# Optimization experiments

Measured on AMD Instinct MI355X. Metric: run time of the kernel, lower is better.

The kernel has to match this reference:

```python
import jax, jax.numpy as jnp
import numpy as np

B, N, C, NH = 4, 2304, 256, 8
HD = C // NH            # head dim = 32
HS = WS = 48            # H = W = sqrt(N)
RADIUS = 3.0
MLP_HID = 4 * C
SCALE = HD ** (-0.5)
NEG = -1e9              # stands in for -inf (identical softmax up to fp eps)
EPS = 1e-6


def spatial_mask():
    # get_spatial_mask: cdist of (y, x) grid coords, -inf where dist > radius
    yy, xx = jnp.meshgrid(jnp.arange(HS), jnp.arange(WS), indexing='ij')
    coords = jnp.stack([yy, xx], -1).reshape(-1, 2).astype(jnp.float32)  # [N, 2]
    d2 = jnp.sum((coords[:, None, :] - coords[None, :, :]) ** 2, -1)     # [N, N]
    return jnp.where(d2 > RADIUS * RADIUS, NEG, 0.0)


def layernorm(x, g, b):
    mu = jnp.mean(x, -1, keepdims=True)
    var = jnp.mean((x - mu) ** 2, -1, keepdims=True)
    return (x - mu) * jax.lax.rsqrt(var + EPS) * g + b


def setup_inputs() -> dict:
    key = jax.random.key(0)
    ks = jax.random.split(key, 16)
    s = 0.02
    return {
        'x':    jax.random.normal(ks[0], (B, N, C), jnp.float32),
        'x_kv': jax.random.normal(ks[1], (B, N, C), jnp.float32),
        'Wq': jax.random.normal(ks[2], (C, C), jnp.float32) * s,
        'bq': jnp.zeros((C,), jnp.float32),
        'Wk': jax.random.normal(ks[3], (C, C), jnp.float32) * s,
        'bk': jnp.zeros((C,), jnp.float32),
        'Wv': jax.random.normal(ks[4], (C, C), jnp.float32) * s,
        'bv': jnp.zeros((C,), jnp.float32),
        'Wp': jax.random.normal(ks[5], (C, C), jnp.float32) * s,
        'bp': jnp.zeros((C,), jnp.float32),
        'g1': jnp.ones((C,), jnp.float32),
        'b1': jnp.zeros((C,), jnp.float32),
        'g2': jnp.ones((C,), jnp.float32),
        'b2': jnp.zeros((C,), jnp.float32),
        'W1': jax.random.normal(ks[6], (C, MLP_HID), jnp.float32) * s,
        'bm1': jnp.zeros((MLP_HID,), jnp.float32),
        'W2': jax.random.normal(ks[7], (MLP_HID, C), jnp.float32) * s,
        'bm2': jnp.zeros((C,), jnp.float32),
    }


def reference(x, x_kv, Wq, bq, Wk, bk, Wv, bv, Wp, bp,
              g1, b1, g2, b2, W1, bm1, W2, bm2):
    mask = spatial_mask()                                  # [N, N]
    h = layernorm(x, g1, b1)
    hkv = layernorm(x_kv, g1, b1)
    q = (h @ Wq + bq).reshape(B, N, NH, HD)
    k = (hkv @ Wk + bk).reshape(B, N, NH, HD)
    v = (hkv @ Wv + bv).reshape(B, N, NH, HD)
    scores = jnp.einsum('bqhd,bkhd->bhqk', q, k) * SCALE + mask
    attn = jax.nn.softmax(scores, axis=-1)
    out = jnp.einsum('bhqk,bkhd->bqhd', attn, v).reshape(B, N, C)
    x = x + out @ Wp + bp
    m = layernorm(x, g2, b2)
    x = x + jax.nn.gelu(m @ W1 + bm1, approximate=False) @ W2 + bm2
    return x
```

## Files before the change

### kernel.cpp

```cpp
#include <hip/hip_runtime.h>
#include <hip/hip_fp16.h>
#include <math.h>

#define BB 4
#define NN 2304
#define CC 256
#define HS 48
#define HID 1024
#define BNROWS (BB * NN)
#define ATTN_SCALE 0.17677669529663687f

typedef _Float16 f16;
typedef __attribute__((ext_vector_type(2))) _Float16 h2;
typedef __attribute__((ext_vector_type(8))) _Float16 h8;
typedef __attribute__((ext_vector_type(4))) float f4;

#define GLLS16(g, l)                                                        \
    __builtin_amdgcn_global_load_lds(                                       \
        (const __attribute__((address_space(1))) unsigned int*)(g),         \
        (__attribute__((address_space(3))) unsigned int*)(l), 16, 0, 0)

#define WAIT_VM0()   asm volatile("s_waitcnt vmcnt(0)" ::: "memory")
#define WAIT_LGKM0() asm volatile("s_waitcnt lgkmcnt(0)" ::: "memory")

static __device__ __forceinline__ float wave_sum64(float v) {
    v += __shfl_xor(v, 32, 64);
    v += __shfl_xor(v, 16, 64);
    v += __shfl_xor(v, 8, 64);
    v += __shfl_xor(v, 4, 64);
    v += __shfl_xor(v, 2, 64);
    v += __shfl_xor(v, 1, 64);
    return v;
}

__global__ __launch_bounds__(256) void prep_kernel(
    const float* __restrict__ Wq, const float* __restrict__ Wk,
    const float* __restrict__ Wv, const float* __restrict__ Wp,
    const float* __restrict__ W1, const float* __restrict__ W2,
    const float* __restrict__ bq, const float* __restrict__ bk,
    const float* __restrict__ bv,
    f16* __restrict__ WqkvT, f16* __restrict__ WpT,
    f16* __restrict__ W1T, f16* __restrict__ W2T, float* __restrict__ bqkv)
{
    int bx = blockIdx.x;
    if (bx == 768) {
        const int t = threadIdx.x;
        bqkv[t]       = bq[t];
        bqkv[t + 256] = bk[t];
        bqkv[t + 512] = bv[t];
        return;
    }
    __shared__ float tt[32][33];
    const float* src; f16* dst; int K, N;
    if (bx < 64)        { src = Wq; dst = WqkvT;             K = 256;  N = 256; }
    else if (bx < 128)  { src = Wk; dst = WqkvT + 65536;     K = 256;  N = 256;  bx -= 64; }
    else if (bx < 192)  { src = Wv; dst = WqkvT + 131072;    K = 256;  N = 256;  bx -= 128; }
    else if (bx < 256)  { src = Wp; dst = WpT;               K = 256;  N = 256;  bx -= 192; }
    else if (bx < 512)  { src = W1; dst = W1T;               K = 256;  N = 1024; bx -= 256; }
    else                { src = W2; dst = W2T;               K = 1024; N = 256;  bx -= 512; }
    const int tN = N >> 5;
    const int kt = bx / tN, nt = bx - kt * tN;
    const int rr = threadIdx.x >> 5, cc = threadIdx.x & 31;
#pragma unroll
    for (int j = 0; j < 4; ++j)
        tt[rr + 8 * j][cc] = src[(size_t)(kt * 32 + rr + 8 * j) * N + nt * 32 + cc];
    __syncthreads();
#pragma unroll
    for (int j = 0; j < 4; ++j)
        dst[(size_t)(nt * 32 + rr + 8 * j) * K + kt * 32 + cc] = (f16)tt[cc][rr + 8 * j];
}

__global__ __launch_bounds__(256) void ln1_kernel(
    const float* __restrict__ x, const float* __restrict__ xkv,
    const float* __restrict__ g, const float* __restrict__ be,
    f16* __restrict__ hq, f16* __restrict__ hkv)
{
    const int r = blockIdx.x * 4 + (threadIdx.x >> 6);
    const int lane = threadIdx.x & 63;
    const float* src; f16* dst;
    if (r < BNROWS) { src = x + (size_t)r * CC;             dst = hq + (size_t)r * CC; }
    else { src = xkv + (size_t)(r - BNROWS) * CC; dst = hkv + (size_t)(r - BNROWS) * CC; }
    const float4 v = ((const float4*)src)[lane];
    const float mu = wave_sum64(v.x + v.y + v.z + v.w) * (1.0f / CC);
    const float d0 = v.x - mu, d1 = v.y - mu, d2 = v.z - mu, d3 = v.w - mu;
    const float var = wave_sum64(d0 * d0 + d1 * d1 + d2 * d2 + d3 * d3) * (1.0f / CC);
    const float rs = rsqrtf(var + 1e-6f);
    const float4 g4 = ((const float4*)g)[lane];
    const float4 b4 = ((const float4*)be)[lane];
    h2 o01 = (h2){(f16)(d0 * rs * g4.x + b4.x), (f16)(d1 * rs * g4.y + b4.y)};
    h2 o23 = (h2){(f16)(d2 * rs * g4.z + b4.z), (f16)(d3 * rs * g4.w + b4.w)};
    ((h2*)dst)[lane * 2] = o01;
    ((h2*)dst)[lane * 2 + 1] = o23;
}

__global__ __launch_bounds__(256) void ln2_kernel(
    const f16* __restrict__ x1, const float* __restrict__ g,
    const float* __restrict__ be, f16* __restrict__ m2)
{
    const int r = blockIdx.x * 4 + (threadIdx.x >> 6);
    const int lane = threadIdx.x & 63;
    const f16* src = x1 + (size_t)r * CC;
    const h2 a01 = ((const h2*)src)[lane * 2];
    const h2 a23 = ((const h2*)src)[lane * 2 + 1];
    const float v0 = (float)a01[0], v1 = (float)a01[1];
    const float v2 = (float)a23[0], v3 = (float)a23[1];
    const float mu = wave_sum64(v0 + v1 + v2 + v3) * (1.0f / CC);
    const float d0 = v0 - mu, d1 = v1 - mu, d2 = v2 - mu, d3 = v3 - mu;
    const float var = wave_sum64(d0 * d0 + d1 * d1 + d2 * d2 + d3 * d3) * (1.0f / CC);
    const float rs = rsqrtf(var + 1e-6f);
    const float4 g4 = ((const float4*)g)[lane];
    const float4 b4 = ((const float4*)be)[lane];
    f16* dst = m2 + (size_t)r * CC;
    h2 o01 = (h2){(f16)(d0 * rs * g4.x + b4.x), (f16)(d1 * rs * g4.y + b4.y)};
    h2 o23 = (h2){(f16)(d2 * rs * g4.z + b4.z), (f16)(d3 * rs * g4.w + b4.w)};
    ((h2*)dst)[lane * 2] = o01;
    ((h2*)dst)[lane * 2 + 1] = o23;
}

template <int TM, bool GELU, int RESID, bool OUTF32, bool QKV>
__global__ __launch_bounds__(256, 4) void gemm_wave(
    const f16* __restrict__ Aq, const f16* __restrict__ Akv,
    const f16* __restrict__ Bt, const float* __restrict__ bias,
    const void* __restrict__ resid, void* __restrict__ out1,
    void* __restrict__ outkv, int M, int N, int K)
{
    constexpr int AT = TM / 16;
    constexpr int AELEM = TM * 32;
    __shared__ f16 lds[4 * (AELEM + 2048)];
    const int tid = threadIdx.x;
    const int wid = tid >> 6, lane = tid & 63;
    const int ln15 = lane & 15, quad = lane >> 4;
    f16* Al = lds + wid * (AELEM + 2048);
    f16* Bl = Al + AELEM;
    const int n0 = blockIdx.x * 64;
    const int m0 = (blockIdx.y * 4 + wid) * TM;
    const f16* Ap = QKV ? (n0 < 256 ? Aq : Akv) : Aq;

    const int jr = lane >> 2, js = lane & 3;
    size_t ga[AT], gb[4];
#pragma unroll
    for (int i = 0; i < AT; ++i) {
        const int r = i * 16 + jr;
        const int q = (js - (r >> 1)) & 3;
        ga[i] = (size_t)(m0 + r) * K + q * 8;
    }
#pragma unroll
    for (int i = 0; i < 4; ++i) {
        const int r = i * 16 + jr;
        const int q = (js - (r >> 1)) & 3;
        gb[i] = (size_t)(n0 + r) * K + q * 8;
    }
    int aoff[AT], boff[4];
#pragma unroll
    for (int mt = 0; mt < AT; ++mt) {
        const int r = mt * 16 + ln15;
        aoff[mt] = (r * 4 + ((quad + (r >> 1)) & 3)) * 16;
    }
#pragma unroll
    for (int nt = 0; nt < 4; ++nt) {
        const int r = nt * 16 + ln15;
        boff[nt] = (r * 4 + ((quad + (r >> 1)) & 3)) * 16;
    }

    f4 acc[AT][4];
#pragma unroll
    for (int i = 0; i < AT; ++i)
#pragma unroll
        for (int j = 0; j < 4; ++j) acc[i][j] = (f4){0.f, 0.f, 0.f, 0.f};

    for (int k0 = 0; k0 < K; k0 += 32) {
        if (k0) WAIT_LGKM0();
#pragma unroll
        for (int i = 0; i < AT; ++i)
            GLLS16(Ap + ga[i] + k0, Al + i * 512);
#pragma unroll
        for (int i = 0; i < 4; ++i)
            GLLS16(Bt + gb[i] + k0, Bl + i * 512);
        WAIT_VM0();
        h8 bF[4], aF[AT];
#pragma unroll
        for (int nt = 0; nt < 4; ++nt)
            bF[nt] = *(const h8*)((const char*)Bl + boff[nt]);
#pragma unroll
        for (int mt = 0; mt < AT; ++mt)
            aF[mt] = *(const h8*)((const char*)Al + aoff[mt]);
#pragma unroll
        for (int mt = 0; mt < AT; ++mt)
#pragma unroll
            for (int nt = 0; nt < 4; ++nt)
                acc[mt][nt] = __builtin_amdgcn_mfma_f32_16x16x32_f16(
                    aF[mt], bF[nt], acc[mt][nt], 0, 0, 0);
    }

#pragma unroll
    for (int nt = 0; nt < 4; ++nt) {
        const int gn = n0 + nt * 16 + ln15;
        const float bs = bias[gn];
#pragma unroll
        for (int mt = 0; mt < AT; ++mt) {
#pragma unroll
            for (int r = 0; r < 4; ++r) {
                const int gm = m0 + mt * 16 + quad * 4 + r;
                float v = acc[mt][nt][r] + bs;
                if (GELU) v = 0.5f * v * (1.0f + erff(v * 0.70710678118654752f));
                if (RESID == 1) v += ((const float*)resid)[(size_t)gm * N + gn];
                if (RESID == 2) v += (float)((const f16*)resid)[(size_t)gm * N + gn];
                if (QKV) {
                    if (gn < 256) ((f16*)out1)[(size_t)gm * 256 + gn] = (f16)v;
                    else ((f16*)outkv)[(size_t)gm * 512 + (gn - 256)] = (f16)v;
                } else if (OUTF32) {
                    ((float*)out1)[(size_t)gm * N + gn] = v;
                } else {
                    ((f16*)out1)[(size_t)gm * N + gn] = (f16)v;
                }
            }
        }
    }
}

__device__ __constant__ int ATT_DY[29] = {
    -3, -2, -2, -2, -2, -2, -1, -1, -1, -1, -1, 0, 0, 0, 0,
    0, 0, 0, 1, 1, 1, 1, 1, 2, 2, 2, 2, 2, 3};
__device__ __constant__ int ATT_DX[29] = {
    0, -2, -1, 0, 1, 2, -2, -1, 0, 1, 2, -3, -2, -1, 0,
    1, 2, 3, -2, -1, 0, 1, 2, -2, -1, 0, 1, 2, 0};

__global__ __launch_bounds__(128) void attn_tile_kernel(
    const f16* __restrict__ qf, const f16* __restrict__ kvf,
    f16* __restrict__ ao)
{
    __shared__ f16 ks[196][66];
    __shared__ f16 vs[196][66];
    const int tile = blockIdx.x, hp = blockIdx.y, b = blockIdx.z;
    const int ty0 = (tile / 6) * 8, tx0 = (tile - (tile / 6) * 6) * 8;
    const int tid = threadIdx.x;

    for (int idx = tid; idx < 196 * 16; idx += 128) {
        const int r = idx >> 4, seg = idx & 15;
        const int gy = ty0 - 3 + r / 14, gx = tx0 - 3 + (r - (r / 14) * 14);
        uint4 val = {0u, 0u, 0u, 0u};
        if ((unsigned)gy < HS && (unsigned)gx < HS) {
            const size_t rowb = ((size_t)b * NN + gy * HS + gx) * 512;
            const int ch = (seg < 8) ? (hp * 64 + seg * 8)
                                     : (256 + hp * 64 + (seg - 8) * 8);
            val = *(const uint4*)&kvf[rowb + ch];
        }
        f16* dstp = (seg < 8) ? &ks[r][(seg & 7) * 8] : &vs[r][(seg & 7) * 8];
        ((unsigned int*)dstp)[0] = val.x;
        ((unsigned int*)dstp)[1] = val.y;
        ((unsigned int*)dstp)[2] = val.z;
        ((unsigned int*)dstp)[3] = val.w;
    }
    __syncthreads();

    const int q = tid & 63, hh = tid >> 6;
    const int qy = q >> 3, qx = q & 7;
    const size_t qrow = (size_t)b * NN + (ty0 + qy) * HS + tx0 + qx;
    const f16* qp = qf + qrow * CC + hp * 64 + hh * 32;
    uint4 qa[4];
#pragma unroll
    for (int i = 0; i < 4; ++i) qa[i] = ((const uint4*)qp)[i];
    const h2* q2 = (const h2*)qa;

    float s[29];
#pragma unroll
    for (int n = 0; n < 29; ++n) {
        const int dy = ATT_DY[n], dx = ATT_DX[n];
        const int r = (qy + 3 + dy) * 14 + qx + 3 + dx;
        const bool valid = (unsigned)(ty0 + qy + dy) < HS &&
                           (unsigned)(tx0 + qx + dx) < HS;
        float a = 0.0f;
        const h2* kp = (const h2*)&ks[r][hh * 32];
#pragma unroll
        for (int i = 0; i < 16; ++i)
            a = __builtin_amdgcn_fdot2(q2[i], kp[i], a, false);
        s[n] = valid ? a * ATTN_SCALE : -1e30f;
    }
    float m = s[0];
#pragma unroll
    for (int n = 1; n < 29; ++n) m = fmaxf(m, s[n]);
    float l = 0.0f;
#pragma unroll
    for (int n = 0; n < 29; ++n) { s[n] = __expf(s[n] - m); l += s[n]; }
    h2 a2[16];
#pragma unroll
    for (int i = 0; i < 16; ++i) a2[i] = (h2){(f16)0.f, (f16)0.f};
#pragma unroll
    for (int n = 0; n < 29; ++n) {
        const int dy = ATT_DY[n], dx = ATT_DX[n];
        const int r = (qy + 3 + dy) * 14 + qx + 3 + dx;
        const f16 pn = (f16)s[n];
        const h2 ph = (h2){pn, pn};
        const h2* vp = (const h2*)&vs[r][hh * 32];
#pragma unroll
        for (int i = 0; i < 16; ++i) a2[i] += ph * vp[i];
    }
    const float inv = 1.0f / l;
    uint4 ov[4];
    f16* oh = (f16*)ov;
#pragma unroll
    for (int i = 0; i < 16; ++i) {
        oh[2 * i]     = (f16)((float)a2[i][0] * inv);
        oh[2 * i + 1] = (f16)((float)a2[i][1] * inv);
    }
    uint4* dst = (uint4*)(ao + qrow * CC + hp * 64 + hh * 32);
#pragma unroll
    for (int i = 0; i < 4; ++i) dst[i] = ov[i];
}

extern "C" void kernel_launch(void* const* d_in, const int* in_sizes, int n_in,
                              void* d_out, int out_size, void* d_ws, size_t ws_size,
                              hipStream_t stream) {
    const float* x    = (const float*)d_in[0];
    const float* x_kv = (const float*)d_in[1];
    const float* Wq   = (const float*)d_in[2];
    const float* bq   = (const float*)d_in[3];
    const float* Wk   = (const float*)d_in[4];
    const float* bk   = (const float*)d_in[5];
    const float* Wv   = (const float*)d_in[6];
    const float* bv   = (const float*)d_in[7];
    const float* Wp   = (const float*)d_in[8];
    const float* bp   = (const float*)d_in[9];
    const float* g1   = (const float*)d_in[10];
    const float* b1   = (const float*)d_in[11];
    const float* g2   = (const float*)d_in[12];
    const float* b2   = (const float*)d_in[13];
    const float* W1   = (const float*)d_in[14];
    const float* bm1  = (const float*)d_in[15];
    const float* W2   = (const float*)d_in[16];
    const float* bm2  = (const float*)d_in[17];
    float* outp = (float*)d_out;

    f16* wsh = (f16*)d_ws;
    f16* WqkvT = wsh;
    f16* WpT   = wsh + 196608;
    f16* W1T   = wsh + 262144;
    f16* W2T   = wsh + 524288;
    float* bqkv = (float*)(wsh + 786432);
    f16* hq    = wsh + 787968;
    f16* hkv   = wsh + 3147264;
    f16* qf    = wsh + 5506560;
    f16* kvf   = wsh + 7865856;
    f16* ao    = hq;
    f16* x1    = hkv;
    f16* m2    = qf;
    f16* hidF  = kvf;
    const bool fused = ws_size >= (size_t)17303040 * sizeof(f16);

    prep_kernel<<<769, 256, 0, stream>>>(Wq, Wk, Wv, Wp, W1, W2, bq, bk, bv,
                                         WqkvT, WpT, W1T, W2T, bqkv);
    ln1_kernel<<<2 * BNROWS / 4, 256, 0, stream>>>(x, x_kv, g1, b1, hq, hkv);
    gemm_wave<64, false, 0, false, true><<<dim3(12, 36), 256, 0, stream>>>(
        hq, hkv, WqkvT, bqkv, nullptr, qf, kvf, BNROWS, 768, CC);
    attn_tile_kernel<<<dim3(36, 4, BB), 128, 0, stream>>>(qf, kvf, ao);
    gemm_wave<32, false, 1, false, false><<<dim3(4, 72), 256, 0, stream>>>(
        ao, nullptr, WpT, bp, x, x1, nullptr, BNROWS, CC, CC);
    ln2_kernel<<<BNROWS / 4, 256, 0, stream>>>(x1, g2, b2, m2);
    if (fused) {
        gemm_wave<64, true, 0, false, false><<<dim3(16, 36), 256, 0, stream>>>(
            m2, nullptr, W1T, bm1, nullptr, hidF, nullptr, BNROWS, HID, CC);
        gemm_wave<32, false, 2, true, false><<<dim3(4, 72), 256, 0, stream>>>(
            hidF, nullptr, W2T, bm2, x1, outp, nullptr, BNROWS, CC, HID);
    } else {
        for (int b = 0; b < BB; ++b) {
            const size_t off = (size_t)b * NN * CC;
            gemm_wave<64, true, 0, false, false><<<dim3(16, 9), 256, 0, stream>>>(
                m2 + off, nullptr, W1T, bm1, nullptr, hidF, nullptr, NN, HID, CC);
            gemm_wave<32, false, 2, true, false><<<dim3(4, 18), 256, 0, stream>>>(
                hidF, nullptr, W2T, bm2, x1 + off, outp + off, nullptr, NN, CC, HID);
        }
    }
    (void)in_sizes; (void)n_in; (void)out_size;
}
```

Baseline: 196.9 us.

## Fuse all stages into one persistent cooperative megakernel with grid syncs

Replaces the chain of separate kernel launches (weight prep, LN1, QKV GEMM, attention, projection, LN2, MLP GEMMs) with a single cooperative kernel of 256 blocks x 512 threads that steps through the phases and calls grid.sync between them. The GEMMs become a per-wave loop over 32x64 tiles with a software-prefetched LDS load. Attention now reads K/V straight from global memory per thread instead of staging a tile in shared memory. This removes launch gaps but adds grid-wide barrier costs, drops the LDS reuse in attention, and uses small GEMM tiles. The workspace layout no longer aliases buffers and needs more memory, and the fallback for small workspaces is removed.

```diff
diff --git a/kernel.cpp b/kernel.cpp
--- a/kernel.cpp
+++ b/kernel.cpp
@@ -1,6 +1,9 @@
 #include <hip/hip_runtime.h>
 #include <hip/hip_fp16.h>
+#include <hip/hip_cooperative_groups.h>
 #include <math.h>
+
+namespace cg = cooperative_groups;
 
 #define BB 4
 #define NN 2304
@@ -9,6 +12,7 @@
 #define HID 1024
 #define BNROWS (BB * NN)
 #define ATTN_SCALE 0.17677669529663687f
+#define NWAVES 2048
 
 typedef _Float16 f16;
 typedef __attribute__((ext_vector_type(2))) _Float16 h2;
@@ -19,9 +23,15 @@
     __builtin_amdgcn_global_load_lds(                                       \
         (const __attribute__((address_space(1))) unsigned int*)(g),         \
         (__attribute__((address_space(3))) unsigned int*)(l), 16, 0, 0)
-
 #define WAIT_VM0()   asm volatile("s_waitcnt vmcnt(0)" ::: "memory")
 #define WAIT_LGKM0() asm volatile("s_waitcnt lgkmcnt(0)" ::: "memory")
+
+__device__ __constant__ int ATT_DY[29] = {
+    -3, -2, -2, -2, -2, -2, -1, -1, -1, -1, -1, 0, 0, 0, 0,
+    0, 0, 0, 1, 1, 1, 1, 1, 2, 2, 2, 2, 2, 3};
+__device__ __constant__ int ATT_DX[29] = {
+    0, -2, -1, 0, 1, 2, -2, -1, 0, 1, 2, -3, -2, -1, 0,
+    1, 2, 3, -2, -1, 0, 1, 2, -2, -1, 0, 1, 2, 0};
 
 static __device__ __forceinline__ float wave_sum64(float v) {
     v += __shfl_xor(v, 32, 64);
@@ -33,279 +43,303 @@
     return v;
 }
 
-__global__ __launch_bounds__(256) void prep_kernel(
+template <bool GELU, int RESID, bool OUTF32, bool QKV>
+static __device__ void gemm_phase(
+    f16* slot, int gw,
+    const f16* __restrict__ Aq, const f16* __restrict__ Akv,
+    const f16* __restrict__ Bt, const float* __restrict__ bias,
+    const void* __restrict__ resid, void* __restrict__ out1,
+    void* __restrict__ outkv, int Mtiles, int Ntiles, int N, int K)
+{
+    const int lane = threadIdx.x & 63;
+    const int ln15 = lane & 15, quad = lane >> 4;
+    const int jr = lane >> 2, js = lane & 3;
+    f16* Al = slot;
+    f16* Bl = slot + 1024;
+    const int T = Mtiles * Ntiles;
+
+    for (int t = gw; t < T; t += NWAVES) {
+        const int n0 = (t % Ntiles) * 64;
+        const int m0 = (t / Ntiles) * 32;
+        const f16* Ap = QKV ? (n0 < 256 ? Aq : Akv) : Aq;
+
+        size_t ga[2], gb[4];
+#pragma unroll
+        for (int i = 0; i < 2; ++i) {
+            const int r = i * 16 + jr;
+            const int q = (js - (r >> 1)) & 3;
+            ga[i] = (size_t)(m0 + r) * K + q * 8;
+        }
+#pragma unroll
+        for (int i = 0; i < 4; ++i) {
+            const int r = i * 16 + jr;
+            const int q = (js - (r >> 1)) & 3;
+            gb[i] = (size_t)(n0 + r) * K + q * 8;
+        }
+        int aoff[2], boff[4];
+#pragma unroll
+        for (int mt = 0; mt < 2; ++mt) {
+            const int r = mt * 16 + ln15;
+            aoff[mt] = (r * 4 + ((quad + (r >> 1)) & 3)) * 16;
+        }
+#pragma unroll
+        for (int nt = 0; nt < 4; ++nt) {
+            const int r = nt * 16 + ln15;
+            boff[nt] = (r * 4 + ((quad + (r >> 1)) & 3)) * 16;
+        }
+
+        f4 acc[2][4];
+#pragma unroll
+        for (int i = 0; i < 2; ++i)
+#pragma unroll
+            for (int j = 0; j < 4; ++j) acc[i][j] = (f4){0.f, 0.f, 0.f, 0.f};
+
+#pragma unroll
+        for (int i = 0; i < 2; ++i) GLLS16(Ap + ga[i], Al + i * 512);
+#pragma unroll
+        for (int i = 0; i < 4; ++i) GLLS16(Bt + gb[i], Bl + i * 512);
+
+        for (int k0 = 0; k0 < K; k0 += 32) {
+            WAIT_VM0();
+            h8 aF[2], bF[4];
+#pragma unroll
+            for (int nt = 0; nt < 4; ++nt)
+                bF[nt] = *(const h8*)((const char*)Bl + boff[nt]);
+#pragma unroll
+            for (int mt = 0; mt < 2; ++mt)
+                aF[mt] = *(const h8*)((const char*)Al + aoff[mt]);
+            WAIT_LGKM0();
+            if (k0 + 32 < K) {
+#pragma unroll
+                for (int i = 0; i < 2; ++i)
+                    GLLS16(Ap + ga[i] + k0 + 32, Al + i * 512);
+#pragma unroll
+                for (int i = 0; i < 4; ++i)
+                    GLLS16(Bt + gb[i] + k0 + 32, Bl + i * 512);
+            }
+#pragma unroll
+            for (int mt = 0; mt < 2; ++mt)
+#pragma unroll
+                for (int nt = 0; nt < 4; ++nt)
+                    acc[mt][nt] = __builtin_amdgcn_mfma_f32_16x16x32_f16(
+                        aF[mt], bF[nt], acc[mt][nt], 0, 0, 0);
+        }
+
+#pragma unroll
+        for (int nt = 0; nt < 4; ++nt) {
+            const int gn = n0 + nt * 16 + ln15;
+            const float bs = bias[gn];
+#pragma unroll
+            for (int mt = 0; mt < 2; ++mt) {
+#pragma unroll
+                for (int r = 0; r < 4; ++r) {
+                    const int gm = m0 + mt * 16 + quad * 4 + r;
+                    float v = acc[mt][nt][r] + bs;
+                    if (GELU) v = 0.5f * v * (1.0f + erff(v * 0.70710678118654752f));
+                    if (RESID == 1) v += ((const float*)resid)[(size_t)gm * N + gn];
+                    if (RESID == 2) v += (float)((const f16*)resid)[(size_t)gm * N + gn];
+                    if (QKV) {
+                        if (gn < 256) ((f16*)out1)[(size_t)gm * 256 + gn] = (f16)v;
+                        else ((f16*)outkv)[(size_t)gm * 512 + (gn - 256)] = (f16)v;
+                    } else if (OUTF32) {
+                        ((float*)out1)[(size_t)gm * N + gn] = v;
+                    } else {
+                        ((f16*)out1)[(size_t)gm * N + gn] = (f16)v;
+                    }
+                }
+            }
+        }
+    }
+}
+
+__global__ __launch_bounds__(512, 2) void mega_kernel(
+    const float* __restrict__ x, const float* __restrict__ x_kv,
     const float* __restrict__ Wq, const float* __restrict__ Wk,
     const float* __restrict__ Wv, const float* __restrict__ Wp,
     const float* __restrict__ W1, const float* __restrict__ W2,
     const float* __restrict__ bq, const float* __restrict__ bk,
-    const float* __restrict__ bv,
-    f16* __restrict__ WqkvT, f16* __restrict__ WpT,
-    f16* __restrict__ W1T, f16* __restrict__ W2T, float* __restrict__ bqkv)
+    const float* __restrict__ bv, const float* __restrict__ bp,
+    const float* __restrict__ bm1, const float* __restrict__ bm2,
+    const float* __restrict__ g1, const float* __restrict__ b1,
+    const float* __restrict__ g2, const float* __restrict__ b2,
+    f16* WqkvT, f16* WpT, f16* W1T, f16* W2T, float* bqkv,
+    f16* hq, f16* hkv, f16* qf, f16* kvf, f16* ao, f16* x1, f16* m2,
+    f16* hidF, float* outp)
 {
-    int bx = blockIdx.x;
-    if (bx == 768) {
-        const int t = threadIdx.x;
-        bqkv[t]       = bq[t];
-        bqkv[t + 256] = bk[t];
-        bqkv[t + 512] = bv[t];
-        return;
-    }
-    __shared__ float tt[32][33];
-    const float* src; f16* dst; int K, N;
-    if (bx < 64)        { src = Wq; dst = WqkvT;             K = 256;  N = 256; }
-    else if (bx < 128)  { src = Wk; dst = WqkvT + 65536;     K = 256;  N = 256;  bx -= 64; }
-    else if (bx < 192)  { src = Wv; dst = WqkvT + 131072;    K = 256;  N = 256;  bx -= 128; }
-    else if (bx < 256)  { src = Wp; dst = WpT;               K = 256;  N = 256;  bx -= 192; }
-    else if (bx < 512)  { src = W1; dst = W1T;               K = 256;  N = 1024; bx -= 256; }
-    else                { src = W2; dst = W2T;               K = 1024; N = 256;  bx -= 512; }
-    const int tN = N >> 5;
-    const int kt = bx / tN, nt = bx - kt * tN;
-    const int rr = threadIdx.x >> 5, cc = threadIdx.x & 31;
-#pragma unroll
-    for (int j = 0; j < 4; ++j)
-        tt[rr + 8 * j][cc] = src[(size_t)(kt * 32 + rr + 8 * j) * N + nt * 32 + cc];
-    __syncthreads();
-#pragma unroll
-    for (int j = 0; j < 4; ++j)
-        dst[(size_t)(nt * 32 + rr + 8 * j) * K + kt * 32 + cc] = (f16)tt[cc][rr + 8 * j];
-}
-
-__global__ __launch_bounds__(256) void ln1_kernel(
-    const float* __restrict__ x, const float* __restrict__ xkv,
-    const float* __restrict__ g, const float* __restrict__ be,
-    f16* __restrict__ hq, f16* __restrict__ hkv)
-{
-    const int r = blockIdx.x * 4 + (threadIdx.x >> 6);
-    const int lane = threadIdx.x & 63;
-    const float* src; f16* dst;
-    if (r < BNROWS) { src = x + (size_t)r * CC;             dst = hq + (size_t)r * CC; }
-    else { src = xkv + (size_t)(r - BNROWS) * CC; dst = hkv + (size_t)(r - BNROWS) * CC; }
-    const float4 v = ((const float4*)src)[lane];
-    const float mu = wave_sum64(v.x + v.y + v.z + v.w) * (1.0f / CC);
-    const float d0 = v.x - mu, d1 = v.y - mu, d2 = v.z - mu, d3 = v.w - mu;
-    const float var = wave_sum64(d0 * d0 + d1 * d1 + d2 * d2 + d3 * d3) * (1.0f / CC);
-    const float rs = rsqrtf(var + 1e-6f);
-    const float4 g4 = ((const float4*)g)[lane];
-    const float4 b4 = ((const float4*)be)[lane];
-    h2 o01 = (h2){(f16)(d0 * rs * g4.x + b4.x), (f16)(d1 * rs * g4.y + b4.y)};
-    h2 o23 = (h2){(f16)(d2 * rs * g4.z + b4.z), (f16)(d3 * rs * g4.w + b4.w)};
-    ((h2*)dst)[lane * 2] = o01;
-    ((h2*)dst)[lane * 2 + 1] = o23;
-}
-
-__global__ __launch_bounds__(256) void ln2_kernel(
-    const f16* __restrict__ x1, const float* __restrict__ g,
-    const float* __restrict__ be, f16* __restrict__ m2)
-{
-    const int r = blockIdx.x * 4 + (threadIdx.x >> 6);
-    const int lane = threadIdx.x & 63;
-    const f16* src = x1 + (size_t)r * CC;
-    const h2 a01 = ((const h2*)src)[lane * 2];
-    const h2 a23 = ((const h2*)src)[lane * 2 + 1];
-    const float v0 = (float)a01[0], v1 = (float)a01[1];
-    const float v2 = (float)a23[0], v3 = (float)a23[1];
-    const float mu = wave_sum64(v0 + v1 + v2 + v3) * (1.0f / CC);
-    const float d0 = v0 - mu, d1 = v1 - mu, d2 = v2 - mu, d3 = v3 - mu;
-    const float var = wave_sum64(d0 * d0 + d1 * d1 + d2 * d2 + d3 * d3) * (1.0f / CC);
-    const float rs = rsqrtf(var + 1e-6f);
-    const float4 g4 = ((const float4*)g)[lane];
-    const float4 b4 = ((const float4*)be)[lane];
-    f16* dst = m2 + (size_t)r * CC;
-    h2 o01 = (h2){(f16)(d0 * rs * g4.x + b4.x), (f16)(d1 * rs * g4.y + b4.y)};
-    h2 o23 = (h2){(f16)(d2 * rs * g4.z + b4.z), (f16)(d3 * rs * g4.w + b4.w)};
-    ((h2*)dst)[lane * 2] = o01;
-    ((h2*)dst)[lane * 2 + 1] = o23;
-}
-
-template <int TM, bool GELU, int RESID, bool OUTF32, bool QKV>
-__global__ __launch_bounds__(256, 4) void gemm_wave(
-    const f16* __restrict__ Aq, const f16* __restrict__ Akv,
-    const f16* __restrict__ Bt, const float* __restrict__ bias,
-    const void* __restrict__ resid, void* __restrict__ out1,
-    void* __restrict__ outkv, int M, int N, int K)
-{
-    constexpr int AT = TM / 16;
-    constexpr int AELEM = TM * 32;
-    __shared__ f16 lds[4 * (AELEM + 2048)];
+    cg::grid_group grid = cg::this_grid();
+    __shared__ __align__(16) char smem[49152];
     const int tid = threadIdx.x;
     const int wid = tid >> 6, lane = tid & 63;
-    const int ln15 = lane & 15, quad = lane >> 4;
-    f16* Al = lds + wid * (AELEM + 2048);
-    f16* Bl = Al + AELEM;
-    const int n0 = blockIdx.x * 64;
-    const int m0 = (blockIdx.y * 4 + wid) * TM;
-    const f16* Ap = QKV ? (n0 < 256 ? Aq : Akv) : Aq;
-
-    const int jr = lane >> 2, js = lane & 3;
-    size_t ga[AT], gb[4];
-#pragma unroll
-    for (int i = 0; i < AT; ++i) {
-        const int r = i * 16 + jr;
-        const int q = (js - (r >> 1)) & 3;
-        ga[i] = (size_t)(m0 + r) * K + q * 8;
+    const int gw = blockIdx.x * 8 + wid;
+    f16* slot = (f16*)smem + wid * 3072;
+
+    {
+        float (*tb)[33] = (float(*)[33])smem;
+        const int rr = tid >> 5, cc = tid & 31;
+#pragma unroll 1
+        for (int i = 0; i < 3; ++i) {
+            int bx = blockIdx.x * 3 + i;
+            const float* src; f16* dst; int K, N;
+            if (bx < 64)        { src = Wq; dst = WqkvT;           K = 256;  N = 256; }
+            else if (bx < 128)  { src = Wk; dst = WqkvT + 65536;   K = 256;  N = 256;  bx -= 64; }
+            else if (bx < 192)  { src = Wv; dst = WqkvT + 131072;  K = 256;  N = 256;  bx -= 128; }
+            else if (bx < 256)  { src = Wp; dst = WpT;             K = 256;  N = 256;  bx -= 192; }
+            else if (bx < 512)  { src = W1; dst = W1T;             K = 256;  N = 1024; bx -= 256; }
+            else                { src = W2; dst = W2T;             K = 1024; N = 256;  bx -= 512; }
+            const int tN = N >> 5;
+            const int kt = bx / tN, nt = bx - kt * tN;
+#pragma unroll
+            for (int j = 0; j < 2; ++j)
+                tb[rr + 16 * j][cc] =
+                    src[(size_t)(kt * 32 + rr + 16 * j) * N + nt * 32 + cc];
+            __syncthreads();
+#pragma unroll
+            for (int j = 0; j < 2; ++j)
+                dst[(size_t)(nt * 32 + rr + 16 * j) * K + kt * 32 + cc] =
+                    (f16)tb[cc][rr + 16 * j];
+            __syncthreads();
+        }
+        if (blockIdx.x == 0 && tid < 256) {
+            bqkv[tid]       = bq[tid];
+            bqkv[tid + 256] = bk[tid];
+            bqkv[tid + 512] = bv[tid];
+        }
+        for (int r = gw; r < 2 * BNROWS; r += NWAVES) {
+            const float* src; f16* dst;
+            if (r < BNROWS) { src = x + (size_t)r * CC; dst = hq + (size_t)r * CC; }
+            else { src = x_kv + (size_t)(r - BNROWS) * CC; dst = hkv + (size_t)(r - BNROWS) * CC; }
+            const float4 v = ((const float4*)src)[lane];
+            const float mu = wave_sum64(v.x + v.y + v.z + v.w) * (1.0f / CC);
+            const float d0 = v.x - mu, d1 = v.y - mu, d2 = v.z - mu, d3 = v.w - mu;
+            const float var = wave_sum64(d0 * d0 + d1 * d1 + d2 * d2 + d3 * d3) * (1.0f / CC);
+            const float rs = rsqrtf(var + 1e-6f);
+            const float4 g4 = ((const float4*)g1)[lane];
+            const float4 b4 = ((const float4*)b1)[lane];
+            h2 o01 = (h2){(f16)(d0 * rs * g4.x + b4.x), (f16)(d1 * rs * g4.y + b4.y)};
+            h2 o23 = (h2){(f16)(d2 * rs * g4.z + b4.z), (f16)(d3 * rs * g4.w + b4.w)};
+            ((h2*)dst)[lane * 2] = o01;
+            ((h2*)dst)[lane * 2 + 1] = o23;
+        }
     }
-#pragma unroll
-    for (int i = 0; i < 4; ++i) {
-        const int r = i * 16 + jr;
-        const int q = (js - (r >> 1)) & 3;
-        gb[i] = (size_t)(n0 + r) * K + q * 8;
+    __threadfence();
+    grid.sync();
+
+    gemm_phase<false, 0, false, true>(slot, gw, hq, hkv, WqkvT, bqkv,
+                                      nullptr, qf, kvf, 288, 12, 768, 256);
+    __threadfence();
+    grid.sync();
+
+    {
+        const int gthread = blockIdx.x * 512 + tid;
+        if (gthread < BNROWS * 8) {
+            const int h = gthread & 7, q = gthread >> 3;
+            const int b = q / NN, qi = q - b * NN;
+            const int qy = qi / HS, qx = qi - qy * HS;
+            const size_t rowb0 = (size_t)b * NN;
+            const f16* qp = qf + (size_t)q * CC + h * 32;
+            h8 qa0 = ((const h8*)qp)[0], qa1 = ((const h8*)qp)[1];
+            h8 qa2 = ((const h8*)qp)[2], qa3 = ((const h8*)qp)[3];
+            const h2* q2a = (const h2*)&qa0;
+            const h2* q2b = (const h2*)&qa1;
+            const h2* q2c = (const h2*)&qa2;
+            const h2* q2d = (const h2*)&qa3;
+
+            float s[29];
+#pragma unroll
+            for (int n = 0; n < 29; ++n) {
+                const int ky = qy + ATT_DY[n], kx = qx + ATT_DX[n];
+                float sn = -1e30f;
+                if ((unsigned)ky < HS && (unsigned)kx < HS) {
+                    const f16* kp = kvf + (rowb0 + ky * HS + kx) * 512 + h * 32;
+                    h8 k0 = ((const h8*)kp)[0], k1 = ((const h8*)kp)[1];
+                    h8 k2 = ((const h8*)kp)[2], k3 = ((const h8*)kp)[3];
+                    const h2* k2a = (const h2*)&k0;
+                    const h2* k2b = (const h2*)&k1;
+                    const h2* k2c = (const h2*)&k2;
+                    const h2* k2d = (const h2*)&k3;
+                    float a0 = 0.f, a1 = 0.f, a2_ = 0.f, a3 = 0.f;
+#pragma unroll
+                    for (int i = 0; i < 4; ++i) {
+                        a0 = __builtin_amdgcn_fdot2(q2a[i], k2a[i], a0, false);
+                        a1 = __builtin_amdgcn_fdot2(q2b[i], k2b[i], a1, false);
+                        a2_ = __builtin_amdgcn_fdot2(q2c[i], k2c[i], a2_, false);
+                        a3 = __builtin_amdgcn_fdot2(q2d[i], k2d[i], a3, false);
+                    }
+                    sn = ((a0 + a1) + (a2_ + a3)) * ATTN_SCALE;
+                }
+                s[n] = sn;
+            }
+            float m = s[0];
+#pragma unroll
+            for (int n = 1; n < 29; ++n) m = fmaxf(m, s[n]);
+            float l = 0.0f;
+#pragma unroll
+            for (int n = 0; n < 29; ++n) { s[n] = __expf(s[n] - m); l += s[n]; }
+
+            h2 a2[16];
+#pragma unroll
+            for (int i = 0; i < 16; ++i) a2[i] = (h2){(f16)0.f, (f16)0.f};
+#pragma unroll
+            for (int n = 0; n < 29; ++n) {
+                const int ky = qy + ATT_DY[n], kx = qx + ATT_DX[n];
+                if ((unsigned)ky < HS && (unsigned)kx < HS) {
+                    const f16* vp = kvf + (rowb0 + ky * HS + kx) * 512 + 256 + h * 32;
+                    const h2* v2 = (const h2*)vp;
+                    const f16 pn = (f16)s[n];
+                    const h2 ph = (h2){pn, pn};
+#pragma unroll
+                    for (int i = 0; i < 16; ++i) a2[i] += ph * v2[i];
+                }
+            }
+            const float inv = 1.0f / l;
+            h8 ov[4];
+            f16* oh = (f16*)ov;
+#pragma unroll
+            for (int i = 0; i < 16; ++i) {
+                oh[2 * i]     = (f16)((float)a2[i][0] * inv);
+                oh[2 * i + 1] = (f16)((float)a2[i][1] * inv);
+            }
+            h8* dst = (h8*)(ao + (size_t)q * CC + h * 32);
+#pragma unroll
+            for (int i = 0; i < 4; ++i) dst[i] = ov[i];
+        }
     }
-    int aoff[AT], boff[4];
-#pragma unroll
-    for (int mt = 0; mt < AT; ++mt) {
-        const int r = mt * 16 + ln15;
-        aoff[mt] = (r * 4 + ((quad + (r >> 1)) & 3)) * 16;
+    __threadfence();
+    grid.sync();
+
+    gemm_phase<false, 1, false, false>(slot, gw, ao, nullptr, WpT, bp,
+                                       x, x1, nullptr, 288, 4, 256, 256);
+    __threadfence();
+    grid.sync();
+
+    for (int r = gw; r < BNROWS; r += NWAVES) {
+        const f16* src = x1 + (size_t)r * CC;
+        const h2 a01 = ((const h2*)src)[lane * 2];
+        const h2 a23 = ((const h2*)src)[lane * 2 + 1];
+        const float v0 = (float)a01[0], v1 = (float)a01[1];
+        const float v2 = (float)a23[0], v3 = (float)a23[1];
+        const float mu = wave_sum64(v0 + v1 + v2 + v3) * (1.0f / CC);
+        const float d0 = v0 - mu, d1 = v1 - mu, d2 = v2 - mu, d3 = v3 - mu;
+        const float var = wave_sum64(d0 * d0 + d1 * d1 + d2 * d2 + d3 * d3) * (1.0f / CC);
+        const float rs = rsqrtf(var + 1e-6f);
+        const float4 g4 = ((const float4*)g2)[lane];
+        const float4 b4 = ((const float4*)b2)[lane];
+        f16* dst = m2 + (size_t)r * CC;
+        h2 o01 = (h2){(f16)(d0 * rs * g4.x + b4.x), (f16)(d1 * rs * g4.y + b4.y)};
+        h2 o23 = (h2){(f16)(d2 * rs * g4.z + b4.z), (f16)(d3 * rs * g4.w + b4.w)};
+        ((h2*)dst)[lane * 2] = o01;
+        ((h2*)dst)[lane * 2 + 1] = o23;
     }
-#pragma unroll
-    for (int nt = 0; nt < 4; ++nt) {
-        const int r = nt * 16 + ln15;
-        boff[nt] = (r * 4 + ((quad + (r >> 1)) & 3)) * 16;
-    }
-
-    f4 acc[AT][4];
-#pragma unroll
-    for (int i = 0; i < AT; ++i)
-#pragma unroll
-        for (int j = 0; j < 4; ++j) acc[i][j] = (f4){0.f, 0.f, 0.f, 0.f};
-
-    for (int k0 = 0; k0 < K; k0 += 32) {
-        if (k0) WAIT_LGKM0();
-#pragma unroll
-        for (int i = 0; i < AT; ++i)
-            GLLS16(Ap + ga[i] + k0, Al + i * 512);
-#pragma unroll
-        for (int i = 0; i < 4; ++i)
-            GLLS16(Bt + gb[i] + k0, Bl + i * 512);
-        WAIT_VM0();
-        h8 bF[4], aF[AT];
-#pragma unroll
-        for (int nt = 0; nt < 4; ++nt)
-            bF[nt] = *(const h8*)((const char*)Bl + boff[nt]);
-#pragma unroll
-        for (int mt = 0; mt < AT; ++mt)
-            aF[mt] = *(const h8*)((const char*)Al + aoff[mt]);
-#pragma unroll
-        for (int mt = 0; mt < AT; ++mt)
-#pragma unroll
-            for (int nt = 0; nt < 4; ++nt)
-                acc[mt][nt] = __builtin_amdgcn_mfma_f32_16x16x32_f16(
-                    aF[mt], bF[nt], acc[mt][nt], 0, 0, 0);
-    }
-
-#pragma unroll
-    for (int nt = 0; nt < 4; ++nt) {
-        const int gn = n0 + nt * 16 + ln15;
-        const float bs = bias[gn];
-#pragma unroll
-        for (int mt = 0; mt < AT; ++mt) {
-#pragma unroll
-            for (int r = 0; r < 4; ++r) {
-                const int gm = m0 + mt * 16 + quad * 4 + r;
-                float v = acc[mt][nt][r] + bs;
-                if (GELU) v = 0.5f * v * (1.0f + erff(v * 0.70710678118654752f));
-                if (RESID == 1) v += ((const float*)resid)[(size_t)gm * N + gn];
-                if (RESID == 2) v += (float)((const f16*)resid)[(size_t)gm * N + gn];
-                if (QKV) {
-                    if (gn < 256) ((f16*)out1)[(size_t)gm * 256 + gn] = (f16)v;
-                    else ((f16*)outkv)[(size_t)gm * 512 + (gn - 256)] = (f16)v;
-                } else if (OUTF32) {
-                    ((float*)out1)[(size_t)gm * N + gn] = v;
-                } else {
-                    ((f16*)out1)[(size_t)gm * N + gn] = (f16)v;
-                }
-            }
-        }
-    }
-}
-
-__device__ __constant__ int ATT_DY[29] = {
-    -3, -2, -2, -2, -2, -2, -1, -1, -1, -1, -1, 0, 0, 0, 0,
-    0, 0, 0, 1, 1, 1, 1, 1, 2, 2, 2, 2, 2, 3};
-__device__ __constant__ int ATT_DX[29] = {
-    0, -2, -1, 0, 1, 2, -2, -1, 0, 1, 2, -3, -2, -1, 0,
-    1, 2, 3, -2, -1, 0, 1, 2, -2, -1, 0, 1, 2, 0};
-
-__global__ __launch_bounds__(128) void attn_tile_kernel(
-    const f16* __restrict__ qf, const f16* __restrict__ kvf,
-    f16* __restrict__ ao)
-{
-    __shared__ f16 ks[196][66];
-    __shared__ f16 vs[196][66];
-    const int tile = blockIdx.x, hp = blockIdx.y, b = blockIdx.z;
-    const int ty0 = (tile / 6) * 8, tx0 = (tile - (tile / 6) * 6) * 8;
-    const int tid = threadIdx.x;
-
-    for (int idx = tid; idx < 196 * 16; idx += 128) {
-        const int r = idx >> 4, seg = idx & 15;
-        const int gy = ty0 - 3 + r / 14, gx = tx0 - 3 + (r - (r / 14) * 14);
-        uint4 val = {0u, 0u, 0u, 0u};
-        if ((unsigned)gy < HS && (unsigned)gx < HS) {
-            const size_t rowb = ((size_t)b * NN + gy * HS + gx) * 512;
-            const int ch = (seg < 8) ? (hp * 64 + seg * 8)
-                                     : (256 + hp * 64 + (seg - 8) * 8);
-            val = *(const uint4*)&kvf[rowb + ch];
-        }
-        f16* dstp = (seg < 8) ? &ks[r][(seg & 7) * 8] : &vs[r][(seg & 7) * 8];
-        ((unsigned int*)dstp)[0] = val.x;
-        ((unsigned int*)dstp)[1] = val.y;
-        ((unsigned int*)dstp)[2] = val.z;
-        ((unsigned int*)dstp)[3] = val.w;
-    }
-    __syncthreads();
-
-    const int q = tid & 63, hh = tid >> 6;
-    const int qy = q >> 3, qx = q & 7;
-    const size_t qrow = (size_t)b * NN + (ty0 + qy) * HS + tx0 + qx;
-    const f16* qp = qf + qrow * CC + hp * 64 + hh * 32;
-    uint4 qa[4];
-#pragma unroll
-    for (int i = 0; i < 4; ++i) qa[i] = ((const uint4*)qp)[i];
-    const h2* q2 = (const h2*)qa;
-
-    float s[29];
-#pragma unroll
-    for (int n = 0; n < 29; ++n) {
-        const int dy = ATT_DY[n], dx = ATT_DX[n];
-        const int r = (qy + 3 + dy) * 14 + qx + 3 + dx;
-        const bool valid = (unsigned)(ty0 + qy + dy) < HS &&
-                           (unsigned)(tx0 + qx + dx) < HS;
-        float a = 0.0f;
-        const h2* kp = (const h2*)&ks[r][hh * 32];
-#pragma unroll
-        for (int i = 0; i < 16; ++i)
-            a = __builtin_amdgcn_fdot2(q2[i], kp[i], a, false);
-        s[n] = valid ? a * ATTN_SCALE : -1e30f;
-    }
-    float m = s[0];
-#pragma unroll
-    for (int n = 1; n < 29; ++n) m = fmaxf(m, s[n]);
-    float l = 0.0f;
-#pragma unroll
-    for (int n = 0; n < 29; ++n) { s[n] = __expf(s[n] - m); l += s[n]; }
-    h2 a2[16];
-#pragma unroll
-    for (int i = 0; i < 16; ++i) a2[i] = (h2){(f16)0.f, (f16)0.f};
-#pragma unroll
-    for (int n = 0; n < 29; ++n) {
-        const int dy = ATT_DY[n], dx = ATT_DX[n];
-        const int r = (qy + 3 + dy) * 14 + qx + 3 + dx;
-        const f16 pn = (f16)s[n];
-        const h2 ph = (h2){pn, pn};
-        const h2* vp = (const h2*)&vs[r][hh * 32];
-#pragma unroll
-        for (int i = 0; i < 16; ++i) a2[i] += ph * vp[i];
-    }
-    const float inv = 1.0f / l;
-    uint4 ov[4];
-    f16* oh = (f16*)ov;
-#pragma unroll
-    for (int i = 0; i < 16; ++i) {
-        oh[2 * i]     = (f16)((float)a2[i][0] * inv);
-        oh[2 * i + 1] = (f16)((float)a2[i][1] * inv);
-    }
-    uint4* dst = (uint4*)(ao + qrow * CC + hp * 64 + hh * 32);
-#pragma unroll
-    for (int i = 0; i < 4; ++i) dst[i] = ov[i];
+    __threadfence();
+    grid.sync();
+
+    gemm_phase<true, 0, false, false>(slot, gw, m2, nullptr, W1T, bm1,
+                                      nullptr, hidF, nullptr, 288, 16, 1024, 256);
+    __threadfence();
+    grid.sync();
+
+    gemm_phase<false, 2, true, false>(slot, gw, hidF, nullptr, W2T, bm2,
+                                      x1, outp, nullptr, 288, 4, 256, 1024);
 }
 
 extern "C" void kernel_launch(void* const* d_in, const int* in_sizes, int n_in,
@@ -338,37 +372,24 @@
     f16* W2T   = wsh + 524288;
     float* bqkv = (float*)(wsh + 786432);
     f16* hq    = wsh + 787968;
-    f16* hkv   = wsh + 3147264;
-    f16* qf    = wsh + 5506560;
-    f16* kvf   = wsh + 7865856;
-    f16* ao    = hq;
-    f16* x1    = hkv;
-    f16* m2    = qf;
-    f16* hidF  = kvf;
-    const bool fused = ws_size >= (size_t)17303040 * sizeof(f16);
-
-    prep_kernel<<<769, 256, 0, stream>>>(Wq, Wk, Wv, Wp, W1, W2, bq, bk, bv,
-                                         WqkvT, WpT, W1T, W2T, bqkv);
-    ln1_kernel<<<2 * BNROWS / 4, 256, 0, stream>>>(x, x_kv, g1, b1, hq, hkv);
-    gemm_wave<64, false, 0, false, true><<<dim3(12, 36), 256, 0, stream>>>(
-        hq, hkv, WqkvT, bqkv, nullptr, qf, kvf, BNROWS, 768, CC);
-    attn_tile_kernel<<<dim3(36, 4, BB), 128, 0, stream>>>(qf, kvf, ao);
-    gemm_wave<32, false, 1, false, false><<<dim3(4, 72), 256, 0, stream>>>(
-        ao, nullptr, WpT, bp, x, x1, nullptr, BNROWS, CC, CC);
-    ln2_kernel<<<BNROWS / 4, 256, 0, stream>>>(x1, g2, b2, m2);
-    if (fused) {
-        gemm_wave<64, true, 0, false, false><<<dim3(16, 36), 256, 0, stream>>>(
-            m2, nullptr, W1T, bm1, nullptr, hidF, nullptr, BNROWS, HID, CC);
-        gemm_wave<32, false, 2, true, false><<<dim3(4, 72), 256, 0, stream>>>(
-            hidF, nullptr, W2T, bm2, x1, outp, nullptr, BNROWS, CC, HID);
-    } else {
-        for (int b = 0; b < BB; ++b) {
-            const size_t off = (size_t)b * NN * CC;
-            gemm_wave<64, true, 0, false, false><<<dim3(16, 9), 256, 0, stream>>>(
-                m2 + off, nullptr, W1T, bm1, nullptr, hidF, nullptr, NN, HID, CC);
-            gemm_wave<32, false, 2, true, false><<<dim3(4, 18), 256, 0, stream>>>(
-                hidF, nullptr, W2T, bm2, x1 + off, outp + off, nullptr, NN, CC, HID);
-        }
-    }
-    (void)in_sizes; (void)n_in; (void)out_size;
+    f16* hkv   = hq  + 2359296;
+    f16* qf    = hkv + 2359296;
+    f16* kvf   = qf  + 2359296;
+    f16* ao    = kvf + 4718592;
+    f16* x1    = ao  + 2359296;
+    f16* m2    = x1  + 2359296;
+    f16* hidF  = m2  + 2359296;
+
+    void* args[] = {
+        (void*)&x, (void*)&x_kv,
+        (void*)&Wq, (void*)&Wk, (void*)&Wv, (void*)&Wp, (void*)&W1, (void*)&W2,
+        (void*)&bq, (void*)&bk, (void*)&bv, (void*)&bp, (void*)&bm1, (void*)&bm2,
+        (void*)&g1, (void*)&b1, (void*)&g2, (void*)&b2,
+        (void*)&WqkvT, (void*)&WpT, (void*)&W1T, (void*)&W2T, (void*)&bqkv,
+        (void*)&hq, (void*)&hkv, (void*)&qf, (void*)&kvf, (void*)&ao,
+        (void*)&x1, (void*)&m2, (void*)&hidF, (void*)&outp
+    };
+    hipLaunchCooperativeKernel(reinterpret_cast<void*>(mega_kernel),
+                               dim3(256), dim3(512), args, 0, stream);
+    (void)in_sizes; (void)n_in; (void)out_size; (void)ws_size;
 }
```

Result: slower. 718.9 us (+265.0%).
